# Optimization experiments

Measured on AMD Instinct MI355X. Metric: run time of the kernel, lower is better.

The kernel has to match this reference:

```python
import jax, jax.numpy as jnp
import numpy as np

B, S, D_MODEL, D_K, D_V, H = 4, 2048, 1024, 1024, 1024, 16


def setup_inputs() -> dict:
    key = jax.random.key(0)
    ks = jax.random.split(key, 8)
    std_qk = np.sqrt(2.0 / (D_MODEL + D_K)).astype(np.float32)
    std_v = np.sqrt(2.0 / (D_MODEL + D_V)).astype(np.float32)
    std_o = np.sqrt(2.0 / (D_V + D_MODEL)).astype(np.float32)  # xavier normal
    return {
        "Q": jax.random.normal(ks[0], (B, S, D_MODEL), jnp.float32),
        "K": jax.random.normal(ks[1], (B, S, D_MODEL), jnp.float32),
        "V": jax.random.normal(ks[2], (B, S, D_MODEL), jnp.float32),
        "Wq": jax.random.normal(ks[3], (D_MODEL, D_K), jnp.float32) * std_qk,
        "bq": jnp.zeros((D_K,), jnp.float32),
        "Wk": jax.random.normal(ks[4], (D_MODEL, D_K), jnp.float32) * std_qk,
        "bk": jnp.zeros((D_K,), jnp.float32),
        "Wv": jax.random.normal(ks[5], (D_MODEL, D_V), jnp.float32) * std_v,
        "bv": jnp.zeros((D_V,), jnp.float32),
        "Wo": jax.random.normal(ks[6], (D_V, D_MODEL), jnp.float32) * std_o,
        "bo": jnp.zeros((D_MODEL,), jnp.float32),
    }


def reference(Q, K, V, Wq, bq, Wk, bk, Wv, bv, Wo, bo):
    b, s, _ = Q.shape
    hd = D_K // H  # per-head dim
    # separate QKV projections
    q = (Q @ Wq + bq).reshape(b, s, H, hd)
    k = (K @ Wk + bk).reshape(b, s, H, hd)
    v = (V @ Wv + bv).reshape(b, s, H, D_V // H)
    # scaled dot-product attention per head
    scale = 1.0 / jnp.sqrt(jnp.asarray(hd, Q.dtype))
    scores = jnp.einsum("bqhd,bkhd->bhqk", q, k) * scale
    attn = jax.nn.softmax(scores, axis=-1)
    o = jnp.einsum("bhqk,bkhd->bqhd", attn, v).reshape(b, s, D_V)
    # output projection
    return o @ Wo + bo
```

## Files before the change

kernel.cpp:

```cpp
#include <hip/hip_runtime.h>
#include <hip/hip_bf16.h>
#include <stdint.h>


#define B_  4
#define S_  2048
#define DM  1024
#define H_  16
#define HD  64
#define BH  (B_ * H_)

typedef __attribute__((ext_vector_type(8))) short short8;
typedef __attribute__((ext_vector_type(4))) float f32x4;

union U8 { short8 v; ushort u[8]; };

__device__ __forceinline__ ushort f2bf(float f) {
  union { float f; uint32_t i; } x; x.f = f;
  uint32_t r = (x.i + 0x7FFFu + ((x.i >> 16) & 1u)) >> 16;
  return (ushort)r;
}

__device__ __forceinline__ uint32_t cvt_pk_bf16(float a, float b) {
  uint32_t r;
  asm("v_cvt_pk_bf16_f32 %0, %1, %2" : "=v"(r) : "v"(a), "v"(b));
  return r;
}

__device__ __forceinline__ float exp2f_fast(float x) {
  float r;
  asm("v_exp_f32 %0, %1" : "=v"(r) : "v"(x));
  return r;
}

__device__ __forceinline__ void glds16(const ushort* g, ushort* l) {
  __builtin_amdgcn_global_load_lds(
      (const __attribute__((address_space(1))) void*)g,
      (__attribute__((address_space(3))) void*)l, 16, 0, 0);
}

#define MAX3(a, b, c) fmaxf(fmaxf((a), (b)), (c))

__global__ __launch_bounds__(256) void transposeW4(
    const float* __restrict__ s0, const float* __restrict__ s1,
    const float* __restrict__ s2, const float* __restrict__ s3,
    ushort* __restrict__ dbase) {
  __shared__ __align__(16) ushort tile[64][72];
  const int t = threadIdx.x;
  const int bx = blockIdx.x & 15;
  const int by = blockIdx.x >> 4;
  const int wsel = blockIdx.y;
  const float* src = wsel == 0 ? s0 : (wsel == 1 ? s1 : (wsel == 2 ? s2 : s3));
  ushort* dst = dbase + (size_t)wsel * 1024 * 1024;
#pragma unroll
  for (int i = 0; i < 2; i++) {
    int e = (i * 256 + t) * 8;
    int r = e >> 6, c = e & 63;
    const float* sp = src + (size_t)(by * 64 + r) * 1024 + bx * 64 + c;
    float4 a = ((const float4*)sp)[0];
    float4 b = ((const float4*)sp)[1];
    tile[r][c + 0] = f2bf(a.x); tile[r][c + 1] = f2bf(a.y);
    tile[r][c + 2] = f2bf(a.z); tile[r][c + 3] = f2bf(a.w);
    tile[r][c + 4] = f2bf(b.x); tile[r][c + 5] = f2bf(b.y);
    tile[r][c + 6] = f2bf(b.z); tile[r][c + 7] = f2bf(b.w);
  }
  __syncthreads();
#pragma unroll
  for (int i = 0; i < 2; i++) {
    int e = (i * 256 + t) * 8;
    int r = e >> 6, c = e & 63;
    U8 st;
#pragma unroll
    for (int j = 0; j < 8; j++) st.u[j] = tile[c + j][r];
    *(short8*)(dst + (size_t)(bx * 64 + r) * 1024 + by * 64 + c) = st.v;
  }
}

template<int AFP32, int CMODE>
__global__ __launch_bounds__(256, 2) void gemm_bt(
    const void* __restrict__ Ap, const ushort* __restrict__ BT,
    const float* __restrict__ bias, void* __restrict__ Cp,
    int M, int N, int K, float oscale) {
  __shared__ __align__(16) ushort lA[128 * 32];
  __shared__ __align__(16) ushort lB[128 * 32];
  const int t = threadIdx.x;
  const int lane = t & 63;
  const int w = t >> 6;
  const int wr = w >> 1, wc = w & 1;
  const int bm0 = blockIdx.x * 128;
  const int bn0 = blockIdx.y * 128;
  f32x4 acc[4][4] = {};

  const int arow = t >> 2;
  const int acol = (t & 3) * 8;
  const ushort* gA0 = (const ushort*)Ap + (size_t)(bm0 + arow) * K + acol;
  const ushort* gA1 = (const ushort*)Ap + (size_t)(bm0 + 64 + arow) * K + acol;
  const float*  fA0 = (const float*)Ap + (size_t)(bm0 + arow) * K + acol;
  const float*  fA1 = (const float*)Ap + (size_t)(bm0 + 64 + arow) * K + acol;
  const ushort* gB0 = BT + (size_t)(bn0 + arow) * K + acol;
  const ushort* gB1 = BT + (size_t)(bn0 + 64 + arow) * K + acol;

  for (int k0 = 0; k0 < K; k0 += 32) {
    if (k0) __syncthreads();
    if constexpr (AFP32) {
      float4 x0 = ((const float4*)(fA0 + k0))[0];
      float4 x1 = ((const float4*)(fA0 + k0))[1];
      float4 y0 = ((const float4*)(fA1 + k0))[0];
      float4 y1 = ((const float4*)(fA1 + k0))[1];
      union { short8 v; uint32_t u[4]; } s0, s1;
      s0.u[0] = cvt_pk_bf16(x0.x, x0.y); s0.u[1] = cvt_pk_bf16(x0.z, x0.w);
      s0.u[2] = cvt_pk_bf16(x1.x, x1.y); s0.u[3] = cvt_pk_bf16(x1.z, x1.w);
      s1.u[0] = cvt_pk_bf16(y0.x, y0.y); s1.u[1] = cvt_pk_bf16(y0.z, y0.w);
      s1.u[2] = cvt_pk_bf16(y1.x, y1.y); s1.u[3] = cvt_pk_bf16(y1.z, y1.w);
      *(short8*)&lA[t * 8] = s0.v;
      *(short8*)&lA[2048 + t * 8] = s1.v;
    } else {
      glds16(gA0 + k0, &lA[t * 8]);
      glds16(gA1 + k0, &lA[2048 + t * 8]);
    }
    glds16(gB0 + k0, &lB[t * 8]);
    glds16(gB1 + k0, &lB[2048 + t * 8]);
    __syncthreads();
    short8 af[4], bf[4];
#pragma unroll
    for (int i = 0; i < 4; i++)
      af[i] = *(const short8*)&lA[(wr * 64 + i * 16 + (lane & 15)) * 32 + (lane >> 4) * 8];
#pragma unroll
    for (int j = 0; j < 4; j++)
      bf[j] = *(const short8*)&lB[(wc * 64 + j * 16 + (lane & 15)) * 32 + (lane >> 4) * 8];
#pragma unroll
    for (int i = 0; i < 4; i++)
#pragma unroll
      for (int j = 0; j < 4; j++)
        acc[i][j] = __builtin_amdgcn_mfma_f32_16x16x32_bf16(af[i], bf[j], acc[i][j], 0, 0, 0);
  }

  const int r0 = (lane >> 4) * 4;
#pragma unroll
  for (int j = 0; j < 4; j++) {
    const int col = bn0 + wc * 64 + j * 16 + (lane & 15);
    const float bc = bias[col];
#pragma unroll
    for (int i = 0; i < 4; i++) {
      const int row = bm0 + wr * 64 + i * 16 + r0;
      if constexpr (CMODE == 2) {
        const int bb = row >> 11, s = row & 2047;
        const int hh = col >> 6, d = col & 63;
        uint32_t p01 = cvt_pk_bf16((acc[i][j][0] + bc) * oscale, (acc[i][j][1] + bc) * oscale);
        uint32_t p23 = cvt_pk_bf16((acc[i][j][2] + bc) * oscale, (acc[i][j][3] + bc) * oscale);
        ushort* vtb = (ushort*)Cp + (((size_t)bb * H_ + hh) * HD + d) * (size_t)S_;
        const int sc = (s & 63) >> 2;
        *(uint2*)(vtb + (s & ~63) + ((sc ^ (d & 15)) << 2)) = (uint2){p01, p23};
      } else {
#pragma unroll
        for (int r = 0; r < 4; r++) {
          float val = (acc[i][j][r] + bc) * oscale;
          if constexpr (CMODE == 0) {
            ((float*)Cp)[(size_t)(row + r) * N + col] = val;
          } else {
            int rr = row + r;
            int b = rr >> 11, s = rr & 2047;
            int h = col >> 6, d = col & 63;
            ((ushort*)Cp)[(((size_t)b * H_ + h) * S_ + s) * HD + d] = f2bf(val);
          }
        }
      }
    }
  }
}

__global__ __launch_bounds__(256, 4) void attn(
    const ushort* __restrict__ q, const ushort* __restrict__ k,
    const ushort* __restrict__ vt, ushort* __restrict__ o) {
  __shared__ __align__(16) ushort kbuf[2][4096];
  __shared__ __align__(16) ushort vbuf[2][4096];
  const int t = threadIdx.x;
  const int lane = t & 63;
  const int w = t >> 6;
  const int L = ((blockIdx.x & 7) << 7) + (blockIdx.x >> 3);
  const int bh = L >> 4;
  const int q0 = (L & 15) * 128;
  const int b = bh >> 4, h = bh & 15;
  const int l15 = lane & 15;
  const int g = lane >> 4;

  const ushort* kbase  = k  + (size_t)bh * S_ * HD;
  const ushort* vtbase = vt + (size_t)bh * HD * S_;

  short8 qf[2][2];
#pragma unroll
  for (int qi = 0; qi < 2; qi++) {
    const ushort* qp = q + ((size_t)bh * S_ + q0 + w * 32 + qi * 16 + l15) * HD + g * 8;
    qf[qi][0] = *(const short8*)qp;
    qf[qi][1] = *(const short8*)(qp + 32);
  }

  short8 onesf;
#pragma unroll
  for (int j = 0; j < 8; j++) onesf[j] = (short)0x3F80;

  float m_r[2] = {-1e30f, -1e30f};
  f32x4 l_acc[2];
  f32x4 o_acc[2][4];
#pragma unroll
  for (int qi = 0; qi < 2; qi++) {
    l_acc[qi] = (f32x4){0.f, 0.f, 0.f, 0.f};
#pragma unroll
    for (int cb = 0; cb < 4; cb++) o_acc[qi][cb] = (f32x4){0.f, 0.f, 0.f, 0.f};
  }

  int vo[2][2];
#pragma unroll
  for (int ks = 0; ks < 2; ks++) {
    vo[ks][0] = ((8 * ks + g) ^ l15) << 2;
    vo[ks][1] = ((8 * ks + 4 + g) ^ l15) << 2;
  }

  auto STAGE = [&](int sel_, int kv0) {
#pragma unroll
    for (int i = 0; i < 2; i++) {
      int c = i * 256 + t;
      int row = c >> 3;
      int cc = (c & 7) ^ (row & 7);
      glds16(kbase + (size_t)(kv0 + row) * HD + cc * 8, &kbuf[sel_][c * 8]);
      glds16(vtbase + (size_t)row * S_ + kv0 + (c & 7) * 8, &vbuf[sel_][c * 8]);
    }
  };

  STAGE(0, 0);
  __syncthreads();

  int sel = 0;
  for (int kv0 = 0; kv0 < S_; kv0 += 64, sel ^= 1) {
    if (kv0 + 64 < S_) STAGE(sel ^ 1, kv0 + 64);

    f32x4 sc[2][4];
#pragma unroll
    for (int qi = 0; qi < 2; qi++)
#pragma unroll
      for (int cb = 0; cb < 4; cb++) sc[qi][cb] = (f32x4){0.f, 0.f, 0.f, 0.f};
    __builtin_amdgcn_s_setprio(1);
#pragma unroll
    for (int cb = 0; cb < 4; cb++) {
      const int row = cb * 16 + l15;
      const int r7 = row & 7;
      short8 kf0 = *(const short8*)&kbuf[sel][(row * 8 + (g ^ r7)) * 8];
      short8 kf1 = *(const short8*)&kbuf[sel][(row * 8 + ((4 + g) ^ r7)) * 8];
#pragma unroll
      for (int qi = 0; qi < 2; qi++) {
        sc[qi][cb] = __builtin_amdgcn_mfma_f32_16x16x32_bf16(kf0, qf[qi][0], sc[qi][cb], 0, 0, 0);
        sc[qi][cb] = __builtin_amdgcn_mfma_f32_16x16x32_bf16(kf1, qf[qi][1], sc[qi][cb], 0, 0, 0);
      }
    }
    __builtin_amdgcn_s_setprio(0);

    union PB { short8 v; uint32_t u[4]; } pbq[2][2];
#pragma unroll
    for (int qi = 0; qi < 2; qi++) {
      const float m = m_r[qi];
#pragma unroll
      for (int cb = 0; cb < 4; cb++) {
        float p0 = exp2f_fast(sc[qi][cb][0] - m);
        float p1 = exp2f_fast(sc[qi][cb][1] - m);
        float p2 = exp2f_fast(sc[qi][cb][2] - m);
        float p3 = exp2f_fast(sc[qi][cb][3] - m);
        pbq[qi][cb >> 1].u[(cb & 1) * 2 + 0] = cvt_pk_bf16(p0, p1);
        pbq[qi][cb >> 1].u[(cb & 1) * 2 + 1] = cvt_pk_bf16(p2, p3);
      }
      float z0 = MAX3(sc[qi][0][0], sc[qi][0][1], sc[qi][0][2]);
      float z1 = MAX3(sc[qi][0][3], sc[qi][1][0], sc[qi][1][1]);
      float z2 = MAX3(sc[qi][1][2], sc[qi][1][3], sc[qi][2][0]);
      float z3 = MAX3(sc[qi][2][1], sc[qi][2][2], sc[qi][2][3]);
      float z4 = MAX3(sc[qi][3][0], sc[qi][3][1], sc[qi][3][2]);
      float mx = MAX3(MAX3(z0, z1, z2), fmaxf(z3, z4), sc[qi][3][3]);
      mx = fmaxf(mx, __shfl_xor(mx, 16));
      mx = fmaxf(mx, __shfl_xor(mx, 32));

      const float THR = 11.5415603f;
      if (!__all(mx <= m + THR)) {
        float mn = fmaxf(m, mx);
        float fct = exp2f_fast(m - mn);
        m_r[qi] = mn;
        l_acc[qi] *= fct;
#pragma unroll
        for (int cb = 0; cb < 4; cb++)
#pragma unroll
          for (int r = 0; r < 4; r++) o_acc[qi][cb][r] *= fct;
#pragma unroll
        for (int cb = 0; cb < 4; cb++) {
          float p0 = exp2f_fast(sc[qi][cb][0] - mn);
          float p1 = exp2f_fast(sc[qi][cb][1] - mn);
          float p2 = exp2f_fast(sc[qi][cb][2] - mn);
          float p3 = exp2f_fast(sc[qi][cb][3] - mn);
          pbq[qi][cb >> 1].u[(cb & 1) * 2 + 0] = cvt_pk_bf16(p0, p1);
          pbq[qi][cb >> 1].u[(cb & 1) * 2 + 1] = cvt_pk_bf16(p2, p3);
        }
      }
    }

    __builtin_amdgcn_s_setprio(1);
#pragma unroll
    for (int qi = 0; qi < 2; qi++) {
#pragma unroll
      for (int ks = 0; ks < 2; ks++) {
        l_acc[qi] = __builtin_amdgcn_mfma_f32_16x16x32_bf16(onesf, pbq[qi][ks].v, l_acc[qi], 0, 0, 0);
#pragma unroll
        for (int cb = 0; cb < 4; cb++) {
          const ushort* vb = &vbuf[sel][(cb * 16 + l15) * 64];
          union { short8 v; uint2 d2[2]; } vv;
          vv.d2[0] = *(const uint2*)(vb + vo[ks][0]);
          vv.d2[1] = *(const uint2*)(vb + vo[ks][1]);
          o_acc[qi][cb] = __builtin_amdgcn_mfma_f32_16x16x32_bf16(vv.v, pbq[qi][ks].v, o_acc[qi][cb], 0, 0, 0);
        }
      }
    }
    __builtin_amdgcn_s_setprio(0);
    __syncthreads();
  }

#pragma unroll
  for (int qi = 0; qi < 2; qi++) {
    const float inv = 1.f / l_acc[qi][0];
    ushort* ob = o + ((size_t)b * S_ + q0 + w * 32 + qi * 16 + l15) * DM + h * HD + 4 * g;
#pragma unroll
    for (int cb = 0; cb < 4; cb++) {
      uint2 st;
      st.x = cvt_pk_bf16(o_acc[qi][cb][0] * inv, o_acc[qi][cb][1] * inv);
      st.y = cvt_pk_bf16(o_acc[qi][cb][2] * inv, o_acc[qi][cb][3] * inv);
      *(uint2*)(ob + cb * 16) = st;
    }
  }
}

extern "C" void kernel_launch(void* const* d_in, const int* in_sizes, int n_in,
                              void* d_out, int out_size, void* d_ws, size_t ws_size,
                              hipStream_t stream) {
  const float* Q  = (const float*)d_in[0];
  const float* K  = (const float*)d_in[1];
  const float* V  = (const float*)d_in[2];
  const float* Wq = (const float*)d_in[3];
  const float* bq = (const float*)d_in[4];
  const float* Wk = (const float*)d_in[5];
  const float* bk = (const float*)d_in[6];
  const float* Wv = (const float*)d_in[7];
  const float* bv = (const float*)d_in[8];
  const float* Wo = (const float*)d_in[9];
  const float* bo = (const float*)d_in[10];
  float* out = (float*)d_out;
  ushort* ws = (ushort*)d_ws;

  const size_t WN = (size_t)1024 * 1024;
  const size_t PN = (size_t)B_ * S_ * DM;
  ushort* wqT = ws;
  ushort* wkT = ws + WN;
  ushort* wvT = ws + 2 * WN;
  ushort* woT = ws + 3 * WN;
  ushort* qws = ws + 4 * WN;
  ushort* kws = qws + PN;
  ushort* ows = kws + PN;
  ushort* vt  = (ushort*)d_out;

  transposeW4<<<dim3(256, 4), 256, 0, stream>>>(Wq, Wk, Wv, Wo, ws);

  dim3 gg(64, 8);
  gemm_bt<1, 1><<<gg, 256, 0, stream>>>(Q, wqT, bq, qws, 8192, 1024, 1024, 0.18033688f);
  gemm_bt<1, 1><<<gg, 256, 0, stream>>>(K, wkT, bk, kws, 8192, 1024, 1024, 1.0f);
  gemm_bt<1, 2><<<gg, 256, 0, stream>>>(V, wvT, bv, vt, 8192, 1024, 1024, 1.0f);

  attn<<<BH * 16, 256, 0, stream>>>(qws, kws, vt, ows);

  gemm_bt<0, 0><<<gg, 256, 0, stream>>>(ows, woT, bo, out, 8192, 1024, 1024, 1.0f);
}
```

Before: 228.2 us.

## Batch QKV projections into one launch and double attention query tile per block

The three separate Q/K/V projection GEMMs become a single launch with blockIdx.z selecting the input, weight, bias and output layout, which gives one larger grid and removes two launches. The attention kernel now processes 256 queries per block (64 per wave) instead of 128, so each staged K/V tile is reused across twice as many queries and the grid shrinks to half as many blocks. Occupancy bounds drop from 4 to 2 blocks per SM to fit the larger accumulator register footprint. The PV loop is also reordered so each V fragment read from LDS feeds four query tiles. The costs are higher register pressure and fewer blocks in flight.

```diff
diff --git a/kernel.cpp b/kernel.cpp
--- a/kernel.cpp
+++ b/kernel.cpp
@@ -76,11 +76,94 @@
   }
 }
 
-template<int AFP32, int CMODE>
-__global__ __launch_bounds__(256, 2) void gemm_bt(
-    const void* __restrict__ Ap, const ushort* __restrict__ BT,
-    const float* __restrict__ bias, void* __restrict__ Cp,
-    int M, int N, int K, float oscale) {
+__global__ __launch_bounds__(256, 2) void gemm_qkv(
+    const float* __restrict__ Qa, const float* __restrict__ Ka, const float* __restrict__ Va,
+    const ushort* __restrict__ WT,
+    const float* __restrict__ bq, const float* __restrict__ bk, const float* __restrict__ bv,
+    ushort* __restrict__ qws, ushort* __restrict__ kws, ushort* __restrict__ vt) {
+  __shared__ __align__(16) ushort lA[128 * 32];
+  __shared__ __align__(16) ushort lB[128 * 32];
+  const int z = blockIdx.z;
+  const float* Ap = z == 0 ? Qa : (z == 1 ? Ka : Va);
+  const ushort* BT = WT + (size_t)z * 1024 * 1024;
+  const float* bias = z == 0 ? bq : (z == 1 ? bk : bv);
+  const float oscale = z == 0 ? 0.18033688f : 1.0f;
+  const int t = threadIdx.x;
+  const int lane = t & 63;
+  const int w = t >> 6;
+  const int wr = w >> 1, wc = w & 1;
+  const int bm0 = blockIdx.x * 128;
+  const int bn0 = blockIdx.y * 128;
+  f32x4 acc[4][4] = {};
+
+  const int arow = t >> 2;
+  const int acol = (t & 3) * 8;
+  const float* fA0 = Ap + (size_t)(bm0 + arow) * 1024 + acol;
+  const float* fA1 = Ap + (size_t)(bm0 + 64 + arow) * 1024 + acol;
+  const ushort* gB0 = BT + (size_t)(bn0 + arow) * 1024 + acol;
+  const ushort* gB1 = BT + (size_t)(bn0 + 64 + arow) * 1024 + acol;
+
+  for (int k0 = 0; k0 < 1024; k0 += 32) {
+    if (k0) __syncthreads();
+    float4 x0 = ((const float4*)(fA0 + k0))[0];
+    float4 x1 = ((const float4*)(fA0 + k0))[1];
+    float4 y0 = ((const float4*)(fA1 + k0))[0];
+    float4 y1 = ((const float4*)(fA1 + k0))[1];
+    union { short8 v; uint32_t u[4]; } s0, s1;
+    s0.u[0] = cvt_pk_bf16(x0.x, x0.y); s0.u[1] = cvt_pk_bf16(x0.z, x0.w);
+    s0.u[2] = cvt_pk_bf16(x1.x, x1.y); s0.u[3] = cvt_pk_bf16(x1.z, x1.w);
+    s1.u[0] = cvt_pk_bf16(y0.x, y0.y); s1.u[1] = cvt_pk_bf16(y0.z, y0.w);
+    s1.u[2] = cvt_pk_bf16(y1.x, y1.y); s1.u[3] = cvt_pk_bf16(y1.z, y1.w);
+    *(short8*)&lA[t * 8] = s0.v;
+    *(short8*)&lA[2048 + t * 8] = s1.v;
+    glds16(gB0 + k0, &lB[t * 8]);
+    glds16(gB1 + k0, &lB[2048 + t * 8]);
+    __syncthreads();
+    short8 af[4], bf[4];
+#pragma unroll
+    for (int i = 0; i < 4; i++)
+      af[i] = *(const short8*)&lA[(wr * 64 + i * 16 + (lane & 15)) * 32 + (lane >> 4) * 8];
+#pragma unroll
+    for (int j = 0; j < 4; j++)
+      bf[j] = *(const short8*)&lB[(wc * 64 + j * 16 + (lane & 15)) * 32 + (lane >> 4) * 8];
+#pragma unroll
+    for (int i = 0; i < 4; i++)
+#pragma unroll
+      for (int j = 0; j < 4; j++)
+        acc[i][j] = __builtin_amdgcn_mfma_f32_16x16x32_bf16(af[i], bf[j], acc[i][j], 0, 0, 0);
+  }
+
+  const int r0 = (lane >> 4) * 4;
+#pragma unroll
+  for (int j = 0; j < 4; j++) {
+    const int col = bn0 + wc * 64 + j * 16 + (lane & 15);
+    const float bc = bias[col];
+#pragma unroll
+    for (int i = 0; i < 4; i++) {
+      const int row = bm0 + wr * 64 + i * 16 + r0;
+      const int bb = row >> 11, s = row & 2047;
+      const int hh = col >> 6, d = col & 63;
+      if (z == 2) {
+        uint32_t p01 = cvt_pk_bf16(acc[i][j][0] + bc, acc[i][j][1] + bc);
+        uint32_t p23 = cvt_pk_bf16(acc[i][j][2] + bc, acc[i][j][3] + bc);
+        ushort* vtb = vt + (((size_t)bb * H_ + hh) * HD + d) * (size_t)S_;
+        const int sc = (s & 63) >> 2;
+        *(uint2*)(vtb + (s & ~63) + ((sc ^ (d & 15)) << 2)) = (uint2){p01, p23};
+      } else {
+        ushort* dst = z == 0 ? qws : kws;
+#pragma unroll
+        for (int r = 0; r < 4; r++) {
+          float val = (acc[i][j][r] + bc) * oscale;
+          dst[(((size_t)bb * H_ + hh) * S_ + (s + r)) * HD + d] = f2bf(val);
+        }
+      }
+    }
+  }
+}
+
+__global__ __launch_bounds__(256, 2) void gemm_out(
+    const ushort* __restrict__ Ap, const ushort* __restrict__ BT,
+    const float* __restrict__ bias, float* __restrict__ Cp) {
   __shared__ __align__(16) ushort lA[128 * 32];
   __shared__ __align__(16) ushort lB[128 * 32];
   const int t = threadIdx.x;
@@ -93,31 +176,15 @@
 
   const int arow = t >> 2;
   const int acol = (t & 3) * 8;
-  const ushort* gA0 = (const ushort*)Ap + (size_t)(bm0 + arow) * K + acol;
-  const ushort* gA1 = (const ushort*)Ap + (size_t)(bm0 + 64 + arow) * K + acol;
-  const float*  fA0 = (const float*)Ap + (size_t)(bm0 + arow) * K + acol;
-  const float*  fA1 = (const float*)Ap + (size_t)(bm0 + 64 + arow) * K + acol;
-  const ushort* gB0 = BT + (size_t)(bn0 + arow) * K + acol;
-  const ushort* gB1 = BT + (size_t)(bn0 + 64 + arow) * K + acol;
-
-  for (int k0 = 0; k0 < K; k0 += 32) {
+  const ushort* gA0 = Ap + (size_t)(bm0 + arow) * 1024 + acol;
+  const ushort* gA1 = Ap + (size_t)(bm0 + 64 + arow) * 1024 + acol;
+  const ushort* gB0 = BT + (size_t)(bn0 + arow) * 1024 + acol;
+  const ushort* gB1 = BT + (size_t)(bn0 + 64 + arow) * 1024 + acol;
+
+  for (int k0 = 0; k0 < 1024; k0 += 32) {
     if (k0) __syncthreads();
-    if constexpr (AFP32) {
-      float4 x0 = ((const float4*)(fA0 + k0))[0];
-      float4 x1 = ((const float4*)(fA0 + k0))[1];
-      float4 y0 = ((const float4*)(fA1 + k0))[0];
-      float4 y1 = ((const float4*)(fA1 + k0))[1];
-      union { short8 v; uint32_t u[4]; } s0, s1;
-      s0.u[0] = cvt_pk_bf16(x0.x, x0.y); s0.u[1] = cvt_pk_bf16(x0.z, x0.w);
-      s0.u[2] = cvt_pk_bf16(x1.x, x1.y); s0.u[3] = cvt_pk_bf16(x1.z, x1.w);
-      s1.u[0] = cvt_pk_bf16(y0.x, y0.y); s1.u[1] = cvt_pk_bf16(y0.z, y0.w);
-      s1.u[2] = cvt_pk_bf16(y1.x, y1.y); s1.u[3] = cvt_pk_bf16(y1.z, y1.w);
-      *(short8*)&lA[t * 8] = s0.v;
-      *(short8*)&lA[2048 + t * 8] = s1.v;
-    } else {
-      glds16(gA0 + k0, &lA[t * 8]);
-      glds16(gA1 + k0, &lA[2048 + t * 8]);
-    }
+    glds16(gA0 + k0, &lA[t * 8]);
+    glds16(gA1 + k0, &lA[2048 + t * 8]);
     glds16(gB0 + k0, &lB[t * 8]);
     glds16(gB1 + k0, &lB[2048 + t * 8]);
     __syncthreads();
@@ -143,33 +210,14 @@
 #pragma unroll
     for (int i = 0; i < 4; i++) {
       const int row = bm0 + wr * 64 + i * 16 + r0;
-      if constexpr (CMODE == 2) {
-        const int bb = row >> 11, s = row & 2047;
-        const int hh = col >> 6, d = col & 63;
-        uint32_t p01 = cvt_pk_bf16((acc[i][j][0] + bc) * oscale, (acc[i][j][1] + bc) * oscale);
-        uint32_t p23 = cvt_pk_bf16((acc[i][j][2] + bc) * oscale, (acc[i][j][3] + bc) * oscale);
-        ushort* vtb = (ushort*)Cp + (((size_t)bb * H_ + hh) * HD + d) * (size_t)S_;
-        const int sc = (s & 63) >> 2;
-        *(uint2*)(vtb + (s & ~63) + ((sc ^ (d & 15)) << 2)) = (uint2){p01, p23};
-      } else {
-#pragma unroll
-        for (int r = 0; r < 4; r++) {
-          float val = (acc[i][j][r] + bc) * oscale;
-          if constexpr (CMODE == 0) {
-            ((float*)Cp)[(size_t)(row + r) * N + col] = val;
-          } else {
-            int rr = row + r;
-            int b = rr >> 11, s = rr & 2047;
-            int h = col >> 6, d = col & 63;
-            ((ushort*)Cp)[(((size_t)b * H_ + h) * S_ + s) * HD + d] = f2bf(val);
-          }
-        }
-      }
-    }
-  }
-}
-
-__global__ __launch_bounds__(256, 4) void attn(
+#pragma unroll
+      for (int r = 0; r < 4; r++)
+        Cp[(size_t)(row + r) * 1024 + col] = acc[i][j][r] + bc;
+    }
+  }
+}
+
+__global__ __launch_bounds__(256, 2) void attn(
     const ushort* __restrict__ q, const ushort* __restrict__ k,
     const ushort* __restrict__ vt, ushort* __restrict__ o) {
   __shared__ __align__(16) ushort kbuf[2][4096];
@@ -177,9 +225,9 @@
   const int t = threadIdx.x;
   const int lane = t & 63;
   const int w = t >> 6;
-  const int L = ((blockIdx.x & 7) << 7) + (blockIdx.x >> 3);
-  const int bh = L >> 4;
-  const int q0 = (L & 15) * 128;
+  const int L = ((blockIdx.x & 7) << 6) + (blockIdx.x >> 3);
+  const int bh = L >> 3;
+  const int q0 = (L & 7) * 256;
   const int b = bh >> 4, h = bh & 15;
   const int l15 = lane & 15;
   const int g = lane >> 4;
@@ -187,10 +235,10 @@
   const ushort* kbase  = k  + (size_t)bh * S_ * HD;
   const ushort* vtbase = vt + (size_t)bh * HD * S_;
 
-  short8 qf[2][2];
-#pragma unroll
-  for (int qi = 0; qi < 2; qi++) {
-    const ushort* qp = q + ((size_t)bh * S_ + q0 + w * 32 + qi * 16 + l15) * HD + g * 8;
+  short8 qf[4][2];
+#pragma unroll
+  for (int qi = 0; qi < 4; qi++) {
+    const ushort* qp = q + ((size_t)bh * S_ + q0 + w * 64 + qi * 16 + l15) * HD + g * 8;
     qf[qi][0] = *(const short8*)qp;
     qf[qi][1] = *(const short8*)(qp + 32);
   }
@@ -199,11 +247,11 @@
 #pragma unroll
   for (int j = 0; j < 8; j++) onesf[j] = (short)0x3F80;
 
-  float m_r[2] = {-1e30f, -1e30f};
-  f32x4 l_acc[2];
-  f32x4 o_acc[2][4];
-#pragma unroll
-  for (int qi = 0; qi < 2; qi++) {
+  float m_r[4] = {-1e30f, -1e30f, -1e30f, -1e30f};
+  f32x4 l_acc[4];
+  f32x4 o_acc[4][4];
+#pragma unroll
+  for (int qi = 0; qi < 4; qi++) {
     l_acc[qi] = (f32x4){0.f, 0.f, 0.f, 0.f};
 #pragma unroll
     for (int cb = 0; cb < 4; cb++) o_acc[qi][cb] = (f32x4){0.f, 0.f, 0.f, 0.f};
@@ -234,9 +282,9 @@
   for (int kv0 = 0; kv0 < S_; kv0 += 64, sel ^= 1) {
     if (kv0 + 64 < S_) STAGE(sel ^ 1, kv0 + 64);
 
-    f32x4 sc[2][4];
-#pragma unroll
-    for (int qi = 0; qi < 2; qi++)
+    f32x4 sc[4][4];
+#pragma unroll
+    for (int qi = 0; qi < 4; qi++)
 #pragma unroll
       for (int cb = 0; cb < 4; cb++) sc[qi][cb] = (f32x4){0.f, 0.f, 0.f, 0.f};
     __builtin_amdgcn_s_setprio(1);
@@ -247,16 +295,16 @@
       short8 kf0 = *(const short8*)&kbuf[sel][(row * 8 + (g ^ r7)) * 8];
       short8 kf1 = *(const short8*)&kbuf[sel][(row * 8 + ((4 + g) ^ r7)) * 8];
 #pragma unroll
-      for (int qi = 0; qi < 2; qi++) {
+      for (int qi = 0; qi < 4; qi++) {
         sc[qi][cb] = __builtin_amdgcn_mfma_f32_16x16x32_bf16(kf0, qf[qi][0], sc[qi][cb], 0, 0, 0);
         sc[qi][cb] = __builtin_amdgcn_mfma_f32_16x16x32_bf16(kf1, qf[qi][1], sc[qi][cb], 0, 0, 0);
       }
     }
     __builtin_amdgcn_s_setprio(0);
 
-    union PB { short8 v; uint32_t u[4]; } pbq[2][2];
-#pragma unroll
-    for (int qi = 0; qi < 2; qi++) {
+    union PB { short8 v; uint32_t u[4]; } pbq[4][2];
+#pragma unroll
+    for (int qi = 0; qi < 4; qi++) {
       const float m = m_r[qi];
 #pragma unroll
       for (int cb = 0; cb < 4; cb++) {
@@ -300,18 +348,19 @@
 
     __builtin_amdgcn_s_setprio(1);
 #pragma unroll
-    for (int qi = 0; qi < 2; qi++) {
-#pragma unroll
-      for (int ks = 0; ks < 2; ks++) {
+    for (int ks = 0; ks < 2; ks++) {
+#pragma unroll
+      for (int qi = 0; qi < 4; qi++)
         l_acc[qi] = __builtin_amdgcn_mfma_f32_16x16x32_bf16(onesf, pbq[qi][ks].v, l_acc[qi], 0, 0, 0);
 #pragma unroll
-        for (int cb = 0; cb < 4; cb++) {
-          const ushort* vb = &vbuf[sel][(cb * 16 + l15) * 64];
-          union { short8 v; uint2 d2[2]; } vv;
-          vv.d2[0] = *(const uint2*)(vb + vo[ks][0]);
-          vv.d2[1] = *(const uint2*)(vb + vo[ks][1]);
+      for (int cb = 0; cb < 4; cb++) {
+        const ushort* vb = &vbuf[sel][(cb * 16 + l15) * 64];
+        union { short8 v; uint2 d2[2]; } vv;
+        vv.d2[0] = *(const uint2*)(vb + vo[ks][0]);
+        vv.d2[1] = *(const uint2*)(vb + vo[ks][1]);
+#pragma unroll
+        for (int qi = 0; qi < 4; qi++)
           o_acc[qi][cb] = __builtin_amdgcn_mfma_f32_16x16x32_bf16(vv.v, pbq[qi][ks].v, o_acc[qi][cb], 0, 0, 0);
-        }
       }
     }
     __builtin_amdgcn_s_setprio(0);
@@ -319,9 +368,9 @@
   }
 
 #pragma unroll
-  for (int qi = 0; qi < 2; qi++) {
+  for (int qi = 0; qi < 4; qi++) {
     const float inv = 1.f / l_acc[qi][0];
-    ushort* ob = o + ((size_t)b * S_ + q0 + w * 32 + qi * 16 + l15) * DM + h * HD + 4 * g;
+    ushort* ob = o + ((size_t)b * S_ + q0 + w * 64 + qi * 16 + l15) * DM + h * HD + 4 * g;
 #pragma unroll
     for (int cb = 0; cb < 4; cb++) {
       uint2 st;
@@ -351,23 +400,18 @@
 
   const size_t WN = (size_t)1024 * 1024;
   const size_t PN = (size_t)B_ * S_ * DM;
-  ushort* wqT = ws;
-  ushort* wkT = ws + WN;
-  ushort* wvT = ws + 2 * WN;
+  ushort* wT  = ws;
   ushort* woT = ws + 3 * WN;
   ushort* qws = ws + 4 * WN;
   ushort* kws = qws + PN;
   ushort* ows = kws + PN;
   ushort* vt  = (ushort*)d_out;
 
-  transposeW4<<<dim3(256, 4), 256, 0, stream>>>(Wq, Wk, Wv, Wo, ws);
-
-  dim3 gg(64, 8);
-  gemm_bt<1, 1><<<gg, 256, 0, stream>>>(Q, wqT, bq, qws, 8192, 1024, 1024, 0.18033688f);
-  gemm_bt<1, 1><<<gg, 256, 0, stream>>>(K, wkT, bk, kws, 8192, 1024, 1024, 1.0f);
-  gemm_bt<1, 2><<<gg, 256, 0, stream>>>(V, wvT, bv, vt, 8192, 1024, 1024, 1.0f);
-
-  attn<<<BH * 16, 256, 0, stream>>>(qws, kws, vt, ows);
-
-  gemm_bt<0, 0><<<gg, 256, 0, stream>>>(ows, woT, bo, out, 8192, 1024, 1024, 1.0f);
-}
+  transposeW4<<<dim3(256, 4), 256, 0, stream>>>(Wq, Wk, Wv, Wo, wT);
+
+  gemm_qkv<<<dim3(64, 8, 3), 256, 0, stream>>>(Q, K, V, wT, bq, bk, bv, qws, kws, vt);
+
+  attn<<<BH * 8, 256, 0, stream>>>(qws, kws, vt, ows);
+
+  gemm_out<<<dim3(64, 8), 256, 0, stream>>>(ows, woT, bo, out);
+}
```

Measured after the change: 196.4 us. -13.9%, faster.

## Double attention query tile per block and prefetch fp32 A tiles in GEMM

Applied to the files above, without the earlier changes.

The attention kernel now processes 256 query rows per block (64 per wave), with 4 query sub-tiles per wave. Each K and V fragment read from LDS is reused across twice as many MFMAs, and the grid is halved. Launch bounds drop to 2 blocks per SM to make room for the extra accumulators. Separately, the fp32-input GEMM loads the next k-step's A data into registers before the MFMA loop, hiding global load latency behind compute at the cost of more registers.

```diff
diff --git a/kernel.cpp b/kernel.cpp
--- a/kernel.cpp
+++ b/kernel.cpp
@@ -100,18 +100,22 @@
   const ushort* gB0 = BT + (size_t)(bn0 + arow) * K + acol;
   const ushort* gB1 = BT + (size_t)(bn0 + 64 + arow) * K + acol;
 
+  float4 px0, px1, py0, py1;
+  if constexpr (AFP32) {
+    px0 = ((const float4*)fA0)[0];
+    px1 = ((const float4*)fA0)[1];
+    py0 = ((const float4*)fA1)[0];
+    py1 = ((const float4*)fA1)[1];
+  }
+
   for (int k0 = 0; k0 < K; k0 += 32) {
     if (k0) __syncthreads();
     if constexpr (AFP32) {
-      float4 x0 = ((const float4*)(fA0 + k0))[0];
-      float4 x1 = ((const float4*)(fA0 + k0))[1];
-      float4 y0 = ((const float4*)(fA1 + k0))[0];
-      float4 y1 = ((const float4*)(fA1 + k0))[1];
       union { short8 v; uint32_t u[4]; } s0, s1;
-      s0.u[0] = cvt_pk_bf16(x0.x, x0.y); s0.u[1] = cvt_pk_bf16(x0.z, x0.w);
-      s0.u[2] = cvt_pk_bf16(x1.x, x1.y); s0.u[3] = cvt_pk_bf16(x1.z, x1.w);
-      s1.u[0] = cvt_pk_bf16(y0.x, y0.y); s1.u[1] = cvt_pk_bf16(y0.z, y0.w);
-      s1.u[2] = cvt_pk_bf16(y1.x, y1.y); s1.u[3] = cvt_pk_bf16(y1.z, y1.w);
+      s0.u[0] = cvt_pk_bf16(px0.x, px0.y); s0.u[1] = cvt_pk_bf16(px0.z, px0.w);
+      s0.u[2] = cvt_pk_bf16(px1.x, px1.y); s0.u[3] = cvt_pk_bf16(px1.z, px1.w);
+      s1.u[0] = cvt_pk_bf16(py0.x, py0.y); s1.u[1] = cvt_pk_bf16(py0.z, py0.w);
+      s1.u[2] = cvt_pk_bf16(py1.x, py1.y); s1.u[3] = cvt_pk_bf16(py1.z, py1.w);
       *(short8*)&lA[t * 8] = s0.v;
       *(short8*)&lA[2048 + t * 8] = s1.v;
     } else {
@@ -121,6 +125,14 @@
     glds16(gB0 + k0, &lB[t * 8]);
     glds16(gB1 + k0, &lB[2048 + t * 8]);
     __syncthreads();
+    if constexpr (AFP32) {
+      if (k0 + 32 < K) {
+        px0 = ((const float4*)(fA0 + k0 + 32))[0];
+        px1 = ((const float4*)(fA0 + k0 + 32))[1];
+        py0 = ((const float4*)(fA1 + k0 + 32))[0];
+        py1 = ((const float4*)(fA1 + k0 + 32))[1];
+      }
+    }
     short8 af[4], bf[4];
 #pragma unroll
     for (int i = 0; i < 4; i++)
@@ -169,7 +181,7 @@
   }
 }
 
-__global__ __launch_bounds__(256, 4) void attn(
+__global__ __launch_bounds__(256, 2) void attn(
     const ushort* __restrict__ q, const ushort* __restrict__ k,
     const ushort* __restrict__ vt, ushort* __restrict__ o) {
   __shared__ __align__(16) ushort kbuf[2][4096];
@@ -177,9 +189,9 @@
   const int t = threadIdx.x;
   const int lane = t & 63;
   const int w = t >> 6;
-  const int L = ((blockIdx.x & 7) << 7) + (blockIdx.x >> 3);
-  const int bh = L >> 4;
-  const int q0 = (L & 15) * 128;
+  const int L = ((blockIdx.x & 7) << 6) + (blockIdx.x >> 3);
+  const int bh = L >> 3;
+  const int q0 = (L & 7) * 256;
   const int b = bh >> 4, h = bh & 15;
   const int l15 = lane & 15;
   const int g = lane >> 4;
@@ -187,10 +199,10 @@
   const ushort* kbase  = k  + (size_t)bh * S_ * HD;
   const ushort* vtbase = vt + (size_t)bh * HD * S_;
 
-  short8 qf[2][2];
-#pragma unroll
-  for (int qi = 0; qi < 2; qi++) {
-    const ushort* qp = q + ((size_t)bh * S_ + q0 + w * 32 + qi * 16 + l15) * HD + g * 8;
+  short8 qf[4][2];
+#pragma unroll
+  for (int qi = 0; qi < 4; qi++) {
+    const ushort* qp = q + ((size_t)bh * S_ + q0 + w * 64 + qi * 16 + l15) * HD + g * 8;
     qf[qi][0] = *(const short8*)qp;
     qf[qi][1] = *(const short8*)(qp + 32);
   }
@@ -199,11 +211,11 @@
 #pragma unroll
   for (int j = 0; j < 8; j++) onesf[j] = (short)0x3F80;
 
-  float m_r[2] = {-1e30f, -1e30f};
-  f32x4 l_acc[2];
-  f32x4 o_acc[2][4];
-#pragma unroll
-  for (int qi = 0; qi < 2; qi++) {
+  float m_r[4] = {-1e30f, -1e30f, -1e30f, -1e30f};
+  f32x4 l_acc[4];
+  f32x4 o_acc[4][4];
+#pragma unroll
+  for (int qi = 0; qi < 4; qi++) {
     l_acc[qi] = (f32x4){0.f, 0.f, 0.f, 0.f};
 #pragma unroll
     for (int cb = 0; cb < 4; cb++) o_acc[qi][cb] = (f32x4){0.f, 0.f, 0.f, 0.f};
@@ -234,9 +246,9 @@
   for (int kv0 = 0; kv0 < S_; kv0 += 64, sel ^= 1) {
     if (kv0 + 64 < S_) STAGE(sel ^ 1, kv0 + 64);
 
-    f32x4 sc[2][4];
-#pragma unroll
-    for (int qi = 0; qi < 2; qi++)
+    f32x4 sc[4][4];
+#pragma unroll
+    for (int qi = 0; qi < 4; qi++)
 #pragma unroll
       for (int cb = 0; cb < 4; cb++) sc[qi][cb] = (f32x4){0.f, 0.f, 0.f, 0.f};
     __builtin_amdgcn_s_setprio(1);
@@ -247,16 +259,16 @@
       short8 kf0 = *(const short8*)&kbuf[sel][(row * 8 + (g ^ r7)) * 8];
       short8 kf1 = *(const short8*)&kbuf[sel][(row * 8 + ((4 + g) ^ r7)) * 8];
 #pragma unroll
-      for (int qi = 0; qi < 2; qi++) {
+      for (int qi = 0; qi < 4; qi++) {
         sc[qi][cb] = __builtin_amdgcn_mfma_f32_16x16x32_bf16(kf0, qf[qi][0], sc[qi][cb], 0, 0, 0);
         sc[qi][cb] = __builtin_amdgcn_mfma_f32_16x16x32_bf16(kf1, qf[qi][1], sc[qi][cb], 0, 0, 0);
       }
     }
     __builtin_amdgcn_s_setprio(0);
 
-    union PB { short8 v; uint32_t u[4]; } pbq[2][2];
-#pragma unroll
-    for (int qi = 0; qi < 2; qi++) {
+    union PB { short8 v; uint32_t u[4]; } pbq[4][2];
+#pragma unroll
+    for (int qi = 0; qi < 4; qi++) {
       const float m = m_r[qi];
 #pragma unroll
       for (int cb = 0; cb < 4; cb++) {
@@ -300,18 +312,19 @@
 
     __builtin_amdgcn_s_setprio(1);
 #pragma unroll
-    for (int qi = 0; qi < 2; qi++) {
-#pragma unroll
-      for (int ks = 0; ks < 2; ks++) {
+    for (int ks = 0; ks < 2; ks++) {
+#pragma unroll
+      for (int qi = 0; qi < 4; qi++)
         l_acc[qi] = __builtin_amdgcn_mfma_f32_16x16x32_bf16(onesf, pbq[qi][ks].v, l_acc[qi], 0, 0, 0);
 #pragma unroll
-        for (int cb = 0; cb < 4; cb++) {
-          const ushort* vb = &vbuf[sel][(cb * 16 + l15) * 64];
-          union { short8 v; uint2 d2[2]; } vv;
-          vv.d2[0] = *(const uint2*)(vb + vo[ks][0]);
-          vv.d2[1] = *(const uint2*)(vb + vo[ks][1]);
+      for (int cb = 0; cb < 4; cb++) {
+        const ushort* vb = &vbuf[sel][(cb * 16 + l15) * 64];
+        union { short8 v; uint2 d2[2]; } vv;
+        vv.d2[0] = *(const uint2*)(vb + vo[ks][0]);
+        vv.d2[1] = *(const uint2*)(vb + vo[ks][1]);
+#pragma unroll
+        for (int qi = 0; qi < 4; qi++)
           o_acc[qi][cb] = __builtin_amdgcn_mfma_f32_16x16x32_bf16(vv.v, pbq[qi][ks].v, o_acc[qi][cb], 0, 0, 0);
-        }
       }
     }
     __builtin_amdgcn_s_setprio(0);
@@ -319,9 +332,9 @@
   }
 
 #pragma unroll
-  for (int qi = 0; qi < 2; qi++) {
+  for (int qi = 0; qi < 4; qi++) {
     const float inv = 1.f / l_acc[qi][0];
-    ushort* ob = o + ((size_t)b * S_ + q0 + w * 32 + qi * 16 + l15) * DM + h * HD + 4 * g;
+    ushort* ob = o + ((size_t)b * S_ + q0 + w * 64 + qi * 16 + l15) * DM + h * HD + 4 * g;
 #pragma unroll
     for (int cb = 0; cb < 4; cb++) {
       uint2 st;
@@ -367,7 +380,7 @@
   gemm_bt<1, 1><<<gg, 256, 0, stream>>>(K, wkT, bk, kws, 8192, 1024, 1024, 1.0f);
   gemm_bt<1, 2><<<gg, 256, 0, stream>>>(V, wvT, bv, vt, 8192, 1024, 1024, 1.0f);
 
-  attn<<<BH * 16, 256, 0, stream>>>(qws, kws, vt, ows);
+  attn<<<BH * 8, 256, 0, stream>>>(qws, kws, vt, ows);
 
   gemm_bt<0, 0><<<gg, 256, 0, stream>>>(ows, woT, bo, out, 8192, 1024, 1024, 1.0f);
 }
```

After: 211.4 us. 1.08x faster.
